# Kernel tuning notes

Measured on AMD Instinct MI355X. Metric: run time of the kernel, lower is better.

## Reference

```python
import jax, jax.numpy as jnp
import numpy as np

ALPHA = 0.2  # LeakyReLU negative slope


def setup_inputs() -> dict:
    key = jax.random.key(0)
    ks = jax.random.split(key, 7)
    B, Wn, K, E, O = 16, 64, 256, 128, 64
    s = lambda k, shape, fan: jax.random.normal(k, shape, jnp.float32) * (1.0 / np.sqrt(fan))
    return {
        "x": jax.random.normal(ks[0], (B, Wn, K), jnp.float32),
        "lin_w": s(ks[1], (E, 2 * Wn), 2 * Wn),   # torch Linear weight (out,in)
        "lin_b": jnp.zeros((E,), jnp.float32),
        "a": s(ks[2], (E,), E),
        "bias_kk": s(ks[3], (K, K), K) * 0.1,
        "fc_w": s(ks[4], (O, K), K),
        "fc_b": jnp.zeros((O,), jnp.float32),
    }


def reference(x, lin_w, lin_b, a, bias_kk, fc_w, fc_b):
    # x: (B, W, K) -> v: (B, K, W); K nodes, W features per node
    v = jnp.transpose(x, (0, 2, 1))
    Wn = v.shape[-1]
    # lin(concat(v_i, v_j)) == v_i @ W1^T + v_j @ W2^T + b  (avoids O(K^2*2W) concat)
    W1, W2 = lin_w[:, :Wn], lin_w[:, Wn:]
    left = jnp.einsum("bkw,ew->bke", v, W1)   # (B,K,E)
    right = jnp.einsum("bkw,ew->bke", v, W2)  # (B,K,E)
    g = left[:, :, None, :] + right[:, None, :, :] + lin_b  # (B,K,K,E)
    g = jnp.where(g >= 0, g, ALPHA * g)  # LeakyReLU
    e = jnp.einsum("bije,e->bij", g, a) + bias_kk  # (B,K,K)
    attn = jax.nn.softmax(e, axis=2)
    # dropout p=0.0 / eval mode -> identity
    h = jax.nn.sigmoid(jnp.einsum("bij,bjw->biw", attn, v))  # (B,K,W)
    out = jnp.einsum("bwk,ok->bwo", jnp.transpose(h, (0, 2, 1)), fc_w) + fc_b
    return out  # (B, W, out_dim)
```

## Files before the change

### kernel.cpp

```cpp
#include <hip/hip_runtime.h>
#include <hip/hip_bf16.h>

#define ALPHA 0.2f
#define C1 0.6f
#define C2 0.4f

typedef const __attribute__((address_space(1))) float gas_float;
typedef __attribute__((address_space(3))) float las_float;

__device__ __forceinline__ void gld_lds16(const float* g, float* l) {
  __builtin_amdgcn_global_load_lds((gas_float*)g, (las_float*)l, 16, 0, 0);
}

__global__ __launch_bounds__(256) void k_proj(
    const float* __restrict__ x, const float* __restrict__ lin_w,
    float* __restrict__ left, float* __restrict__ right, float* __restrict__ v) {
  const int xcd = blockIdx.x & 7;
  const int s   = blockIdx.x >> 3;
  const int b   = 2 * xcd + (s & 1);
  const int k0  = (s >> 1) * 8;
  const int tid = threadIdx.x;

  __shared__ float s_x[8][68];

  {
    const int w  = tid >> 2;
    const int kq = tid & 3;
    float2 xv = *(const float2*)(x + b * 16384 + w * 256 + k0 + kq * 2);
    s_x[kq * 2 + 0][w] = xv.x;
    s_x[kq * 2 + 1][w] = xv.y;
  }
  __syncthreads();

  if (tid < 128) {
    const int k  = tid >> 4;
    const int wq = tid & 15;
    float4 vv = *(const float4*)&s_x[k][wq * 4];
    *(float4*)(v + (b * 256 + k0 + k) * 64 + wq * 4) = vv;
  }

  const int e  = tid & 127;
  const int kh = tid >> 7;
  float accL[4] = {0, 0, 0, 0};
  float accR[4] = {0, 0, 0, 0};
  const float4* w1 = (const float4*)(lin_w + e * 128);
  const float4* w2 = w1 + 16;
#pragma unroll
  for (int wc = 0; wc < 16; ++wc) {
    float4 l = w1[wc];
    float4 r = w2[wc];
#pragma unroll
    for (int k = 0; k < 4; ++k) {
      float4 sx = *(const float4*)&s_x[kh * 4 + k][wc * 4];
      accL[k] += sx.x * l.x + sx.y * l.y + sx.z * l.z + sx.w * l.w;
      accR[k] += sx.x * r.x + sx.y * r.y + sx.z * r.z + sx.w * r.w;
    }
  }
#pragma unroll
  for (int k = 0; k < 4; ++k) {
    int kk = (b * 256 + k0 + kh * 4 + k) * 128 + e;
    left[kk]  = accL[k];
    right[kk] = accR[k];
  }
}

__global__ __launch_bounds__(512, 4) void k_attn(
    const float* __restrict__ left, const float* __restrict__ right,
    const float* __restrict__ lin_b, const float* __restrict__ a,
    const float* __restrict__ bias_kk, const float* __restrict__ v,
    float* __restrict__ h) {
  const int xcd  = blockIdx.x & 7;
  const int sblk = blockIdx.x >> 3;
  const int b    = 2 * xcd + (sblk & 1);
  const int i0   = (sblk >> 1) * 8;
  const int tid  = threadIdx.x;
  const int j    = tid >> 1;
  const int eh   = tid & 1;

  __shared__ float s_lb[8][132];
  __shared__ float s_a[128];
  __shared__ float s_ca[128];
  __shared__ float s_AL[8];
  __shared__ float s_sc[8][260];
  __shared__ float s_v[256][64];

  if (tid < 128) {
    float av = a[tid];
    s_a[tid]  = av;
    s_ca[tid] = C2 * av;
  }
  {
    const int ii = tid >> 6;
    const int e2 = (tid & 63) * 2;
    float2 lv = *(const float2*)(left + (b * 256 + i0 + ii) * 128 + e2);
    float2 bv = *(const float2*)(lin_b + e2);
    s_lb[ii][e2 + 0] = lv.x + bv.x;
    s_lb[ii][e2 + 1] = lv.y + bv.y;
  }
  __syncthreads();

  const float4* rp = (const float4*)(right + (b * 256 + j) * 128 + eh * 64);
  float4 r[16];
#pragma unroll
  for (int q = 0; q < 16; ++q) r[q] = rp[q];

  {
    const int seg0 = (tid >> 6) * 8;
    const int ln4  = (tid & 63) * 4;
    const float* vb = v + b * 16384;
#pragma unroll
    for (int t = 0; t < 8; ++t) {
      const int seg = seg0 + t;
      gld_lds16(vb + seg * 256 + ln4, &s_v[0][0] + seg * 256);
    }
  }

  {
    const int ii = tid >> 6, sl = tid & 63;
    float p = s_a[sl * 2] * s_lb[ii][sl * 2] +
              s_a[sl * 2 + 1] * s_lb[ii][sl * 2 + 1];
#pragma unroll
    for (int off = 32; off > 0; off >>= 1) p += __shfl_xor(p, off, 64);
    if (sl == 0) s_AL[ii] = p;
  }

  float acc[8];
#pragma unroll
  for (int i = 0; i < 8; ++i) acc[i] = 0.f;
  float ar = 0.f;
  const int eb = eh * 64;
#pragma unroll
  for (int ec = 0; ec < 4; ++ec) {
    float4 r0 = r[ec * 4 + 0], r1 = r[ec * 4 + 1],
           r2 = r[ec * 4 + 2], r3 = r[ec * 4 + 3];
    const int base = eb + ec * 16;
    float4 a0 = *(const float4*)&s_a[base + 0];
    float4 a1 = *(const float4*)&s_a[base + 4];
    float4 a2 = *(const float4*)&s_a[base + 8];
    float4 a3 = *(const float4*)&s_a[base + 12];
    ar += a0.x * r0.x + a0.y * r0.y + a0.z * r0.z + a0.w * r0.w;
    ar += a1.x * r1.x + a1.y * r1.y + a1.z * r1.z + a1.w * r1.w;
    ar += a2.x * r2.x + a2.y * r2.y + a2.z * r2.z + a2.w * r2.w;
    ar += a3.x * r3.x + a3.y * r3.y + a3.z * r3.z + a3.w * r3.w;
    float4 c0 = *(const float4*)&s_ca[base + 0];
    float4 c1 = *(const float4*)&s_ca[base + 4];
    float4 c2 = *(const float4*)&s_ca[base + 8];
    float4 c3 = *(const float4*)&s_ca[base + 12];
#pragma unroll
    for (int i = 0; i < 8; ++i) {
      float4 l0 = *(const float4*)&s_lb[i][base + 0];
      float4 l1 = *(const float4*)&s_lb[i][base + 4];
      float4 l2 = *(const float4*)&s_lb[i][base + 8];
      float4 l3 = *(const float4*)&s_lb[i][base + 12];
      float t, s = acc[i];
      t = l0.x + r0.x; s = fmaf(c0.x, fabsf(t), s);
      t = l0.y + r0.y; s = fmaf(c0.y, fabsf(t), s);
      t = l0.z + r0.z; s = fmaf(c0.z, fabsf(t), s);
      t = l0.w + r0.w; s = fmaf(c0.w, fabsf(t), s);
      t = l1.x + r1.x; s = fmaf(c1.x, fabsf(t), s);
      t = l1.y + r1.y; s = fmaf(c1.y, fabsf(t), s);
      t = l1.z + r1.z; s = fmaf(c1.z, fabsf(t), s);
      t = l1.w + r1.w; s = fmaf(c1.w, fabsf(t), s);
      t = l2.x + r2.x; s = fmaf(c2.x, fabsf(t), s);
      t = l2.y + r2.y; s = fmaf(c2.y, fabsf(t), s);
      t = l2.z + r2.z; s = fmaf(c2.z, fabsf(t), s);
      t = l2.w + r2.w; s = fmaf(c2.w, fabsf(t), s);
      t = l3.x + r3.x; s = fmaf(c3.x, fabsf(t), s);
      t = l3.y + r3.y; s = fmaf(c3.y, fabsf(t), s);
      t = l3.z + r3.z; s = fmaf(c3.z, fabsf(t), s);
      t = l3.w + r3.w; s = fmaf(c3.w, fabsf(t), s);
      acc[i] = s;
    }
  }

  float bk[8];
#pragma unroll
  for (int i = 0; i < 8; ++i) bk[i] = bias_kk[(i0 + i) * 256 + j];

  __syncthreads();

#pragma unroll
  for (int i = 0; i < 8; ++i) acc[i] += __shfl_xor(acc[i], 1, 64);
  ar += __shfl_xor(ar, 1, 64);

#pragma unroll
  for (int i = 0; i < 8; ++i) {
    float sc = fmaf(C1, s_AL[i] + ar, acc[i]) + bk[i];
    float p = __expf(sc);
    if (eh == 0) s_sc[i][j] = p;
  }
  __syncthreads();

  float inv;
  {
    const int wv = tid >> 6, lane = tid & 63;
    float ssum = s_sc[wv][lane] + s_sc[wv][lane + 64] +
                 s_sc[wv][lane + 128] + s_sc[wv][lane + 192];
#pragma unroll
    for (int off = 32; off > 0; off >>= 1) ssum += __shfl_xor(ssum, off, 64);
    inv = 1.f / ssum;
  }

  const int iq = tid >> 6;
  const int wp = (tid >> 1) & 31;
  const int jh = tid & 1;
  const int w  = wp * 2;
  float h0 = 0.f, h1 = 0.f;
  const int jbase = jh * 128;
#pragma unroll 4
  for (int jj = 0; jj < 128; jj += 4) {
    float4 at = *(const float4*)&s_sc[iq][jbase + jj];
    float2 v0 = *(const float2*)&s_v[jbase + jj + 0][w];
    float2 v1 = *(const float2*)&s_v[jbase + jj + 1][w];
    float2 v2 = *(const float2*)&s_v[jbase + jj + 2][w];
    float2 v3 = *(const float2*)&s_v[jbase + jj + 3][w];
    h0 += at.x * v0.x + at.y * v1.x + at.z * v2.x + at.w * v3.x;
    h1 += at.x * v0.y + at.y * v1.y + at.z * v2.y + at.w * v3.y;
  }
  h0 += __shfl_xor(h0, 1, 64);
  h1 += __shfl_xor(h1, 1, 64);
  if (jh == 0) {
    float2 hv;
    hv.x = 1.f / (1.f + __expf(-h0 * inv));
    hv.y = 1.f / (1.f + __expf(-h1 * inv));
    *(float2*)(h + (b * 256 + i0 + iq) * 64 + w) = hv;
  }
}

__global__ __launch_bounds__(256) void k_out(
    const float* __restrict__ h, const float* __restrict__ fc_w,
    const float* __restrict__ fc_b, float* __restrict__ out) {
  const int xcd = blockIdx.x & 7;
  const int s   = blockIdx.x >> 3;
  const int b   = 2 * xcd + (s & 1);
  const int wg  = s >> 1;
  const int wl  = threadIdx.x >> 6;
  const int o   = threadIdx.x & 63;
  const int w   = wg * 4 + wl;

  __shared__ float s_h[256 * 4];
  for (int idx = threadIdx.x; idx < 1024; idx += 256) {
    int k = idx >> 2, wl2 = idx & 3;
    s_h[idx] = h[(b * 256 + k) * 64 + wg * 4 + wl2];
  }
  __syncthreads();

  float acc = 0.f;
  const float4* fw = (const float4*)(fc_w + o * 256);
#pragma unroll
  for (int k4 = 0; k4 < 64; ++k4) {
    float4 f = fw[k4];
    int k = k4 * 4;
    acc += s_h[(k + 0) * 4 + wl] * f.x + s_h[(k + 1) * 4 + wl] * f.y +
           s_h[(k + 2) * 4 + wl] * f.z + s_h[(k + 3) * 4 + wl] * f.w;
  }
  out[b * 64 * 64 + w * 64 + o] = acc + fc_b[o];
}

extern "C" void kernel_launch(void* const* d_in, const int* in_sizes, int n_in,
                              void* d_out, int out_size, void* d_ws, size_t ws_size,
                              hipStream_t stream) {
  const float* x       = (const float*)d_in[0];
  const float* lin_w   = (const float*)d_in[1];
  const float* lin_b   = (const float*)d_in[2];
  const float* a       = (const float*)d_in[3];
  const float* bias_kk = (const float*)d_in[4];
  const float* fc_w    = (const float*)d_in[5];
  const float* fc_b    = (const float*)d_in[6];
  float* out = (float*)d_out;

  float* ws    = (float*)d_ws;
  float* left  = ws;
  float* right = ws + 524288;
  float* v     = ws + 1048576;
  float* h     = ws + 1310720;

  k_proj<<<512, 256, 0, stream>>>(x, lin_w, left, right, v);
  k_attn<<<512, 512, 0, stream>>>(left, right, lin_b, a, bias_kk, v, h);
  k_out<<<256, 256, 0, stream>>>(h, fc_w, fc_b, out);
}
```

Measured before the change: 112.4 us.

## Fuse output projection into attention kernel via atomic accumulation

Removes the separate k_out launch. k_attn now computes each block's 8-row slice of h in shared memory, multiplies it by the matching fc_w columns, and atomically adds the partial products into out. k_proj initializes out with fc_b beforehand. This saves one launch and the round trip of h through global memory, but adds 4096 float atomics per block and makes the floating-point summation order nondeterministic.

Result: faster. 104.6 us (-6.9%).

```diff
diff --git a/kernel.cpp b/kernel.cpp
--- a/kernel.cpp
+++ b/kernel.cpp
@@ -14,7 +14,9 @@
 
 __global__ __launch_bounds__(256) void k_proj(
     const float* __restrict__ x, const float* __restrict__ lin_w,
-    float* __restrict__ left, float* __restrict__ right, float* __restrict__ v) {
+    const float* __restrict__ fc_b,
+    float* __restrict__ left, float* __restrict__ right,
+    float* __restrict__ v, float* __restrict__ out) {
   const int xcd = blockIdx.x & 7;
   const int s   = blockIdx.x >> 3;
   const int b   = 2 * xcd + (s & 1);
@@ -22,6 +24,11 @@
   const int tid = threadIdx.x;
 
   __shared__ float s_x[8][68];
+
+  if ((s >> 1) < 16) {
+    const int idx = (s >> 1) * 256 + tid;
+    out[b * 4096 + idx] = fc_b[idx & 63];
+  }
 
   {
     const int w  = tid >> 2;
@@ -68,7 +75,7 @@
     const float* __restrict__ left, const float* __restrict__ right,
     const float* __restrict__ lin_b, const float* __restrict__ a,
     const float* __restrict__ bias_kk, const float* __restrict__ v,
-    float* __restrict__ h) {
+    const float* __restrict__ fc_w, float* __restrict__ out) {
   const int xcd  = blockIdx.x & 7;
   const int sblk = blockIdx.x >> 3;
   const int b    = 2 * xcd + (sblk & 1);
@@ -191,6 +198,9 @@
   }
   __syncthreads();
 
+  const int fo = tid >> 3, fi = tid & 7;
+  float fwv = fc_w[fo * 256 + i0 + fi];
+
   float inv;
   {
     const int wv = tid >> 6, lane = tid & 63;
@@ -219,42 +229,31 @@
   }
   h0 += __shfl_xor(h0, 1, 64);
   h1 += __shfl_xor(h1, 1, 64);
+
+  float* s_h  = &s_lb[0][0];
+  float* s_fw = &s_lb[0][0] + 512;
   if (jh == 0) {
-    float2 hv;
-    hv.x = 1.f / (1.f + __expf(-h0 * inv));
-    hv.y = 1.f / (1.f + __expf(-h1 * inv));
-    *(float2*)(h + (b * 256 + i0 + iq) * 64 + w) = hv;
-  }
-}
-
-__global__ __launch_bounds__(256) void k_out(
-    const float* __restrict__ h, const float* __restrict__ fc_w,
-    const float* __restrict__ fc_b, float* __restrict__ out) {
-  const int xcd = blockIdx.x & 7;
-  const int s   = blockIdx.x >> 3;
-  const int b   = 2 * xcd + (s & 1);
-  const int wg  = s >> 1;
-  const int wl  = threadIdx.x >> 6;
-  const int o   = threadIdx.x & 63;
-  const int w   = wg * 4 + wl;
-
-  __shared__ float s_h[256 * 4];
-  for (int idx = threadIdx.x; idx < 1024; idx += 256) {
-    int k = idx >> 2, wl2 = idx & 3;
-    s_h[idx] = h[(b * 256 + k) * 64 + wg * 4 + wl2];
-  }
-  __syncthreads();
-
-  float acc = 0.f;
-  const float4* fw = (const float4*)(fc_w + o * 256);
-#pragma unroll
-  for (int k4 = 0; k4 < 64; ++k4) {
-    float4 f = fw[k4];
-    int k = k4 * 4;
-    acc += s_h[(k + 0) * 4 + wl] * f.x + s_h[(k + 1) * 4 + wl] * f.y +
-           s_h[(k + 2) * 4 + wl] * f.z + s_h[(k + 3) * 4 + wl] * f.w;
-  }
-  out[b * 64 * 64 + w * 64 + o] = acc + fc_b[o];
+    s_h[iq * 64 + w + 0] = 1.f / (1.f + __expf(-h0 * inv));
+    s_h[iq * 64 + w + 1] = 1.f / (1.f + __expf(-h1 * inv));
+  }
+  s_fw[fi * 64 + fo] = fwv;
+  __syncthreads();
+
+  {
+    const int o   = tid & 63;
+    const int ws8 = (tid >> 6) * 8;
+    float av[8] = {0, 0, 0, 0, 0, 0, 0, 0};
+#pragma unroll
+    for (int i = 0; i < 8; ++i) {
+      float fwi = s_fw[i * 64 + o];
+#pragma unroll
+      for (int ww = 0; ww < 8; ++ww)
+        av[ww] = fmaf(fwi, s_h[i * 64 + ws8 + ww], av[ww]);
+    }
+#pragma unroll
+    for (int ww = 0; ww < 8; ++ww)
+      atomicAdd(&out[b * 4096 + (ws8 + ww) * 64 + o], av[ww]);
+  }
 }
 
 extern "C" void kernel_launch(void* const* d_in, const int* in_sizes, int n_in,
@@ -273,9 +272,7 @@
   float* left  = ws;
   float* right = ws + 524288;
   float* v     = ws + 1048576;
-  float* h     = ws + 1310720;
-
-  k_proj<<<512, 256, 0, stream>>>(x, lin_w, left, right, v);
-  k_attn<<<512, 512, 0, stream>>>(left, right, lin_b, a, bias_kk, v, h);
-  k_out<<<256, 256, 0, stream>>>(h, fc_w, fc_b, out);
-}
+
+  k_proj<<<512, 256, 0, stream>>>(x, lin_w, fc_b, left, right, v, out);
+  k_attn<<<512, 512, 0, stream>>>(left, right, lin_b, a, bias_kk, v, fc_w, out);
+}
```
